# Performance work log

Hardware: AMD Instinct MI355X
Metric: run time of the kernel (lower is better)

## Reference

```python
import jax, jax.numpy as jnp
import numpy as np

GROUPS = 32
EPS = 1e-6


def group_norm(x, gamma, beta):
    b, c, h, w = x.shape
    xg = x.reshape(b, GROUPS, c // GROUPS, h, w)
    mu = xg.mean(axis=(2, 3, 4), keepdims=True)
    var = xg.var(axis=(2, 3, 4), keepdims=True)
    xg = (xg - mu) * jax.lax.rsqrt(var + EPS)
    return xg.reshape(b, c, h, w) * gamma[None, :, None, None] + beta[None, :, None, None]


def conv1x1(x, W, b):
    # 1x1 conv == per-pixel channel GEMM
    return jnp.einsum('oc,bchw->bohw', W, x) + b[None, :, None, None]


def scores(h_, Wq, bq, Wk, bk):
    b, c, H, Wd = h_.shape
    n = H * Wd
    q = conv1x1(h_, Wq, bq).reshape(b, c, n)  # b c n
    k = conv1x1(h_, Wk, bk).reshape(b, c, n)
    # q rearranged to (b, n, c), k to (b, c, n): w_[b,i,j] = sum_c q[b,c,i] k[b,c,j]
    return jnp.einsum('bci,bcj->bij', q, k) * (c ** -0.5)


def proc_attention(v, w_, H, Wd, Wp, bp):
    # w_ already softmaxed over last dim (j). h_[b,c,k] = sum_j v[b,c,j] * w_[b,k,j]
    h_ = jnp.einsum('bkj,bcj->bck', w_, v)
    b, c, _ = h_.shape
    h_ = h_.reshape(b, c, H, Wd)
    return conv1x1(h_, Wp, bp)


def setup_inputs() -> dict:
    key = jax.random.key(0)
    ks = jax.random.split(key, 12)
    B, C, H, W = 8, 256, 48, 48
    s = C ** -0.5
    return {
        'x1': jax.random.normal(ks[0], (B, C, H, W), dtype=jnp.float32),
        'x2': jax.random.normal(ks[1], (B, C, H, W), dtype=jnp.float32),
        'gamma': jnp.ones((C,), jnp.float32),
        'beta': jnp.zeros((C,), jnp.float32),
        'Wq': jax.random.normal(ks[2], (C, C), jnp.float32) * s,
        'bq': jnp.zeros((C,), jnp.float32),
        'Wk': jax.random.normal(ks[3], (C, C), jnp.float32) * s,
        'bk': jnp.zeros((C,), jnp.float32),
        'Wv': jax.random.normal(ks[4], (C, C), jnp.float32) * s,
        'bv': jnp.zeros((C,), jnp.float32),
        'Wp': jax.random.normal(ks[5], (C, C), jnp.float32) * s,
        'bp': jnp.zeros((C,), jnp.float32),
    }


def reference(x1, x2, gamma, beta, Wq, bq, Wk, bk, Wv, bv, Wp, bp):
    b, c, H, Wd = x1.shape
    h1n = group_norm(x1, gamma, beta)
    w1 = scores(h1n, Wq, bq, Wk, bk)                       # [b, n, n]
    v = conv1x1(h1n, Wv, bv).reshape(b, c, H * Wd)          # [b, c, n]
    out_self = x1 + proc_attention(v, jax.nn.softmax(w1, axis=-1), H, Wd, Wp, bp)
    h2n = group_norm(x2, gamma, beta)
    w2 = scores(h2n, Wq, bq, Wk, bk)
    out_cross = x1 + proc_attention(v, jax.nn.softmax(w1 + w2, axis=-1), H, Wd, Wp, bp)
    return (out_self, out_cross)
```

## Files before the change

### kernel.cpp

```cpp
#include <hip/hip_runtime.h>
#include <stdint.h>

typedef unsigned short ushort_t;
typedef __attribute__((ext_vector_type(8))) short bf16x8;
typedef __attribute__((ext_vector_type(4))) float f32x4;
typedef __attribute__((ext_vector_type(16))) float f32x16;
typedef __attribute__((ext_vector_type(4))) unsigned short us4;

static __device__ __forceinline__ unsigned short f2bf(float f) {
  union { float f; uint32_t u; } v; v.f = f;
  uint32_t u = v.u;
  u += 0x7FFFu + ((u >> 16) & 1u);
  return (unsigned short)(u >> 16);
}

static __device__ __forceinline__ float wredsum(float v) {
#pragma unroll
  for (int o = 32; o > 0; o >>= 1) v += __shfl_down(v, o, 64);
  return v;
}

__global__ __launch_bounds__(256) void cvt_w(
    const float* __restrict__ Wq, const float* __restrict__ Wk,
    const float* __restrict__ Wv, const float* __restrict__ Wp,
    ushort_t* __restrict__ dst) {
  int m = blockIdx.y;
  const float* src = (m == 0) ? Wq : (m == 1) ? Wk : (m == 2) ? Wv : Wp;
  int i = blockIdx.x * 256 + threadIdx.x;
  float4 v = ((const float4*)src)[i];
  us4 o;
  o.x = f2bf(v.x); o.y = f2bf(v.y); o.z = f2bf(v.z); o.w = f2bf(v.w);
  *(us4*)&dst[(size_t)m * 65536 + (size_t)i * 4] = o;
}

__global__ __launch_bounds__(512) void pack_bqk(const float* __restrict__ bq,
                                                const float* __restrict__ bk,
                                                float* __restrict__ bqk) {
  int i = threadIdx.x;
  bqk[i] = (i < 256) ? bq[i] : bk[i - 256];
}

__global__ __launch_bounds__(256) void gn_stats(
    const float* __restrict__ x1, const float* __restrict__ x2,
    float* __restrict__ stats) {
  const int sel = blockIdx.x >> 8;
  const int bg = blockIdx.x & 255;
  const float* x = (sel ? x2 : x1) + (size_t)bg * 8 * 2304;
  float s = 0.f, ss = 0.f;
  for (int i = threadIdx.x; i < 4608; i += 256) {
    float4 v = ((const float4*)x)[i];
    s += v.x + v.y + v.z + v.w;
    ss += v.x * v.x + v.y * v.y + v.z * v.z + v.w * v.w;
  }
  s = wredsum(s);
  ss = wredsum(ss);
  __shared__ float ls[8];
  int wave = threadIdx.x >> 6, lane = threadIdx.x & 63;
  if (lane == 0) { ls[wave] = s; ls[4 + wave] = ss; }
  __syncthreads();
  if (threadIdx.x == 0) {
    float S = ls[0] + ls[1] + ls[2] + ls[3];
    float SS = ls[4] + ls[5] + ls[6] + ls[7];
    float mu = S * (1.f / 18432.f);
    float var = SS * (1.f / 18432.f) - mu * mu;
    stats[(sel * 256 + bg) * 2] = mu;
    stats[(sel * 256 + bg) * 2 + 1] = rsqrtf(var + 1e-6f);
  }
}

__global__ __launch_bounds__(256) void gn_apply(
    const float* __restrict__ x1, const float* __restrict__ x2,
    const float* __restrict__ gamma, const float* __restrict__ beta,
    const float* __restrict__ stats,
    ushort_t* __restrict__ h1t, ushort_t* __restrict__ h2t) {
  const int sel = blockIdx.z, b = blockIdx.y, nt = blockIdx.x;
  const int n0 = nt * 64;
  const float* x = (sel ? x2 : x1) + (size_t)b * 256 * 2304;
  ushort_t* ht = (sel ? h2t : h1t) + (size_t)b * 2304 * 256;
  const float* st = stats + (sel * 8 + b) * 64;
  __shared__ ushort_t lt[64 * 260];
#pragma unroll 4
  for (int it = 0; it < 64; ++it) {
    int flat = it * 256 + threadIdx.x;
    int c = flat >> 6, nn = flat & 63;
    float v = x[(size_t)c * 2304 + n0 + nn];
    int g = c >> 3;
    float mu = st[g * 2], rstd = st[g * 2 + 1];
    lt[nn * 260 + c] = f2bf((v - mu) * rstd * gamma[c] + beta[c]);
  }
  __syncthreads();
#pragma unroll 4
  for (int it = 0; it < 16; ++it) {
    int flat4 = it * 256 + threadIdx.x;
    int nn = flat4 >> 6, cq = flat4 & 63;
    us4 vv = *(const us4*)&lt[nn * 260 + cq * 4];
    *(us4*)&ht[(size_t)(n0 + nn) * 256 + cq * 4] = vv;
  }
}

template <int MODE_OUT>
__global__ __launch_bounds__(256) void gemm_bt(
    const ushort_t* __restrict__ Av, const ushort_t* __restrict__ Bv,
    void* __restrict__ Cv, int M, int N, int K, long sA, long sB, long sC,
    const float* __restrict__ bias, const float* __restrict__ res, long sRes,
    void* __restrict__ Cv2) {
  __shared__ ushort_t lA[128 * 32];
  __shared__ ushort_t lB[128 * 32];
  const int tid = threadIdx.x;
  const int lane = tid & 63, wave = tid >> 6;
  const int wm = wave >> 1, wn = wave & 1;
  const int bz = blockIdx.z;
  const int bM = blockIdx.x * 128, bN = blockIdx.y * 128;

  const ushort_t* B = Bv + (size_t)bz * sB + (size_t)bN * K;
  const ushort_t* Ab = Av + (size_t)bz * sA + (size_t)bM * K;

  f32x4 acc[4][4];
#pragma unroll
  for (int m = 0; m < 4; ++m)
#pragma unroll
    for (int n = 0; n < 4; ++n) acc[m][n] = (f32x4){0.f, 0.f, 0.f, 0.f};

  const int nK = K >> 5;
  for (int kt = 0; kt < nK; ++kt) {
    __syncthreads();
#pragma unroll
    for (int i = 0; i < 2; ++i) {
      int c = i * 256 + tid;
      int row = c >> 2, cb = (c & 3) * 8;
      const ushort_t* src = B + (size_t)row * K + kt * 32 + cb;
      __builtin_amdgcn_global_load_lds(
          (const __attribute__((address_space(1))) uint32_t*)src,
          (__attribute__((address_space(3))) uint32_t*)((char*)lB + i * 4096 +
                                                        wave * 1024),
          16, 0, 0);
    }
#pragma unroll
    for (int i = 0; i < 2; ++i) {
      int c = i * 256 + tid;
      int row = c >> 2, cb = (c & 3) * 8;
      const ushort_t* src = Ab + (size_t)row * K + kt * 32 + cb;
      __builtin_amdgcn_global_load_lds(
          (const __attribute__((address_space(1))) uint32_t*)src,
          (__attribute__((address_space(3))) uint32_t*)((char*)lA + i * 4096 +
                                                        wave * 1024),
          16, 0, 0);
    }
    __syncthreads();

    bf16x8 af[4], bfr[4];
    const int ko = (lane >> 4) * 8;
    const int rb = lane & 15;
#pragma unroll
    for (int m = 0; m < 4; ++m)
      af[m] = *(const bf16x8*)&lA[(wm * 64 + m * 16 + rb) * 32 + ko];
#pragma unroll
    for (int n = 0; n < 4; ++n)
      bfr[n] = *(const bf16x8*)&lB[(wn * 64 + n * 16 + rb) * 32 + ko];
#pragma unroll
    for (int m = 0; m < 4; ++m)
#pragma unroll
      for (int n = 0; n < 4; ++n)
        acc[m][n] =
            __builtin_amdgcn_mfma_f32_16x16x32_bf16(af[m], bfr[n], acc[m][n],
                                                    0, 0, 0);
  }

  const int r0 = (lane >> 4) * 4;
  const int c0 = lane & 15;
#pragma unroll
  for (int m = 0; m < 4; ++m) {
#pragma unroll
    for (int n = 0; n < 4; ++n) {
#pragma unroll
      for (int j = 0; j < 4; ++j) {
        int row = bM + wm * 64 + m * 16 + r0 + j;
        int col = bN + wn * 64 + n * 16 + c0;
        float v = acc[m][n][j];
        size_t idx = (size_t)row * N + col;
        if (MODE_OUT == 0) {
          ((ushort_t*)Cv + (size_t)bz * sC)[idx] = f2bf(v + bias[col]);
        } else if (MODE_OUT == 1) {
          ((ushort_t*)Cv + (size_t)bz * sC)[idx] = f2bf(v + bias[row]);
        } else if (MODE_OUT == 5) {
          ((float*)Cv + (size_t)bz * sC)[idx] =
              v + bias[row] + (res + (size_t)bz * sRes)[idx];
        } else if (MODE_OUT == 6) {
          float vv = v + bias[col];
          if (col < 256) {
            ((ushort_t*)Cv + (size_t)bz * sC)[(size_t)row * 256 + col] =
                f2bf(vv);
          } else {
            int cp = col - 256;
            size_t kidx = (size_t)(row >> 6) * 16384 + (size_t)(cp >> 3) * 512 +
                          (size_t)(row & 63) * 8 + (cp & 7);
            ((ushort_t*)Cv2 + (size_t)bz * 589824)[kidx] = f2bf(vv);
          }
        } else if (MODE_OUT == 7) {
          size_t vidx = (size_t)(col >> 6) * 16384 +
                        (size_t)((col >> 3) & 7) * 2048 + (size_t)row * 8 +
                        (col & 7);
          ((ushort_t*)Cv + (size_t)bz * sC)[vidx] = f2bf(v + bias[row]);
        }
      }
    }
  }
}

__global__ __launch_bounds__(256, 2) void flash_attn(
    const ushort_t* __restrict__ q1t, const ushort_t* __restrict__ kf1,
    const ushort_t* __restrict__ q2t, const ushort_t* __restrict__ kf2,
    const ushort_t* __restrict__ vf, ushort_t* __restrict__ att1,
    ushort_t* __restrict__ att2) {
  const int bid = blockIdx.x;
  const int b = bid & 7;
  const int qb = bid >> 3;
  const int tid = threadIdx.x;
  const int lane = tid & 63;
  const int w = tid >> 6;
  const int grp = w >> 1;
  const int wp = w & 1;
  const int l31 = lane & 31;
  const int h = lane >> 5;

  const size_t sH = (size_t)2304 * 256;
  const ushort_t* qp0 = (grp ? q2t : q1t) + b * sH;
  const bf16x8* kb = (const bf16x8*)((grp ? kf2 : kf1) + b * sH);
  const bf16x8* vb = (const bf16x8*)(vf + b * sH);

  __shared__ ushort_t P1[2][32 * 64];
  __shared__ ushort_t P12[32 * 64];
  __shared__ float S1[32 * 64];
  __shared__ float red[2][32];

  bf16x8 qf[16];
  {
    const ushort_t* qp = qp0 + (size_t)(qb * 32 + l31) * 256 + h * 8;
#pragma unroll
    for (int ck = 0; ck < 16; ++ck) qf[ck] = *(const bf16x8*)(qp + ck * 16);
  }

  f32x16 o[4];
#pragma unroll
  for (int cb = 0; cb < 4; ++cb)
#pragma unroll
    for (int r = 0; r < 16; ++r) o[cb][r] = 0.f;
  float lp = 0.f;
  const int iswz = (l31 & 7) << 4;

  auto do_pv = [&](int tt) {
    const ushort_t* pb = grp ? P12 : P1[tt & 1];
    const bf16x8* vt = vb + (size_t)tt * 2048;
#pragma unroll
    for (int jc = 0; jc < 4; ++jc) {
      bf16x8 pa = *(const bf16x8*)((const char*)pb +
                                   ((l31 * 128 + jc * 32 + h * 16) ^ iswz));
#pragma unroll
      for (int cb = 0; cb < 4; ++cb) {
        bf16x8 vfr = vt[(jc * 2 + h) * 256 + wp * 128 + cb * 32 + l31];
        o[cb] =
            __builtin_amdgcn_mfma_f32_32x32x16_bf16(pa, vfr, o[cb], 0, 0, 0);
      }
    }
  };

  f32x16 s2save;
  for (int t = 0; t < 36; ++t) {
    f32x16 s;
#pragma unroll
    for (int r = 0; r < 16; ++r) s[r] = 0.f;
    {
      const bf16x8* kt = kb + (size_t)t * 2048 + wp * 32 + l31;
#pragma unroll
      for (int ck = 0; ck < 16; ++ck) {
        bf16x8 kf = kt[(ck * 2 + h) * 64];
        s = __builtin_amdgcn_mfma_f32_32x32x16_bf16(kf, qf[ck], s, 0, 0, 0);
      }
    }
    if (t > 0) do_pv(t - 1);
    if (grp == 0) {
      float e[16];
#pragma unroll
      for (int r = 0; r < 16; ++r) {
        e[r] = __expf(s[r] * 0.0625f - 8.f);
        lp += e[r];
      }
      char* p1 = (char*)P1[t & 1];
      char* s1 = (char*)S1;
#pragma unroll
      for (int g = 0; g < 4; ++g) {
        uint32_t u0 = (uint32_t)f2bf(e[4 * g]) |
                      ((uint32_t)f2bf(e[4 * g + 1]) << 16);
        uint32_t u1 = (uint32_t)f2bf(e[4 * g + 2]) |
                      ((uint32_t)f2bf(e[4 * g + 3]) << 16);
        *(uint2*)(p1 + ((l31 * 128 + wp * 64 + g * 16 + h * 8) ^ iswz)) =
            make_uint2(u0, u1);
        float4 sv = make_float4(s[4 * g], s[4 * g + 1], s[4 * g + 2],
                                s[4 * g + 3]);
        *(float4*)(s1 + ((l31 * 256 + wp * 128 + g * 32 + h * 16) ^ iswz)) =
            sv;
      }
    } else {
      s2save = s;
    }
    __syncthreads();
    if (grp == 1) {
      const char* s1 = (const char*)S1;
      char* p12 = (char*)P12;
#pragma unroll
      for (int g = 0; g < 4; ++g) {
        float4 sv = *(const float4*)(s1 + ((l31 * 256 + wp * 128 + g * 32 +
                                            h * 16) ^ iswz));
        float e0 = __expf((sv.x + s2save[4 * g + 0]) * 0.0625f - 8.f);
        float e1 = __expf((sv.y + s2save[4 * g + 1]) * 0.0625f - 8.f);
        float e2 = __expf((sv.z + s2save[4 * g + 2]) * 0.0625f - 8.f);
        float e3 = __expf((sv.w + s2save[4 * g + 3]) * 0.0625f - 8.f);
        lp += e0 + e1 + e2 + e3;
        uint32_t u0 = (uint32_t)f2bf(e0) | ((uint32_t)f2bf(e1) << 16);
        uint32_t u1 = (uint32_t)f2bf(e2) | ((uint32_t)f2bf(e3) << 16);
        *(uint2*)(p12 + ((l31 * 128 + wp * 64 + g * 16 + h * 8) ^ iswz)) =
            make_uint2(u0, u1);
      }
    }
    __syncthreads();
  }
  do_pv(35);

  lp += __shfl_xor(lp, 32, 64);
  __syncthreads();
  if (wp == 0 && lane < 32) red[grp][l31] = lp;
  __syncthreads();
  if (wp == 1 && lane < 32) red[grp][l31] += lp;
  __syncthreads();

  ushort_t* ap = (grp ? att2 : att1) + ((size_t)b * 2304 + qb * 32) * 256;
#pragma unroll
  for (int r = 0; r < 16; ++r) {
    int irow = (r & 3) + 8 * (r >> 2) + 4 * h;
    float rl = 1.f / red[grp][irow];
#pragma unroll
    for (int cb = 0; cb < 4; ++cb) {
      int col = wp * 128 + cb * 32 + l31;
      ap[(size_t)irow * 256 + col] = f2bf(o[cb][r] * rl);
    }
  }
}

extern "C" void kernel_launch(void* const* d_in, const int* in_sizes, int n_in,
                              void* d_out, int out_size, void* d_ws,
                              size_t ws_size, hipStream_t stream) {
  (void)in_sizes; (void)n_in; (void)out_size; (void)ws_size;
  const float* x1 = (const float*)d_in[0];
  const float* x2 = (const float*)d_in[1];
  const float* gamma = (const float*)d_in[2];
  const float* beta = (const float*)d_in[3];
  const float* Wq = (const float*)d_in[4];
  const float* bq = (const float*)d_in[5];
  const float* Wk = (const float*)d_in[6];
  const float* bk = (const float*)d_in[7];
  const float* Wv = (const float*)d_in[8];
  const float* bv = (const float*)d_in[9];
  const float* Wp = (const float*)d_in[10];
  const float* bp = (const float*)d_in[11];
  float* out = (float*)d_out;

  const int C = 256, N = 2304;
  const long sH = (long)N * C;
  const long sX = (long)C * N;
  const size_t HE = (size_t)8 * N * C;

  char* ws = (char*)d_ws;
  ushort_t* Wbf = (ushort_t*)ws;
  float* stats = (float*)(ws + 524288);
  float* bqk = (float*)(ws + 528384);
  ushort_t* h1t = (ushort_t*)(ws + 532480);
  ushort_t* h2t = h1t + HE;
  ushort_t* q1t = h2t + HE;
  ushort_t* q2t = q1t + HE;
  ushort_t* kf1 = q2t + HE;
  ushort_t* kf2 = kf1 + HE;
  ushort_t* vfB = kf2 + HE;
  ushort_t* att1 = vfB + HE;
  ushort_t* att2 = att1 + HE;

  cvt_w<<<dim3(64, 4), 256, 0, stream>>>(Wq, Wk, Wv, Wp, Wbf);
  pack_bqk<<<1, 512, 0, stream>>>(bq, bk, bqk);
  gn_stats<<<512, 256, 0, stream>>>(x1, x2, stats);
  gn_apply<<<dim3(36, 8, 2), 256, 0, stream>>>(x1, x2, gamma, beta, stats, h1t,
                                               h2t);

  gemm_bt<6><<<dim3(18, 4, 8), 256, 0, stream>>>(h1t, Wbf, q1t, N, 512, C, sH,
                                                 0, sH, bqk, nullptr, 0, kf1);
  gemm_bt<6><<<dim3(18, 4, 8), 256, 0, stream>>>(h2t, Wbf, q2t, N, 512, C, sH,
                                                 0, sH, bqk, nullptr, 0, kf2);
  gemm_bt<7><<<dim3(2, 18, 8), 256, 0, stream>>>(Wbf + 2 * 65536, h1t, vfB, C,
                                                 N, C, 0, sH, sH, bv, nullptr,
                                                 0, nullptr);

  flash_attn<<<576, 256, 0, stream>>>(q1t, kf1, q2t, kf2, vfB, att1, att2);

  const size_t half = (size_t)8 * C * N;
  gemm_bt<5><<<dim3(2, 18, 8), 256, 0, stream>>>(Wbf + 3 * 65536, att1, out, C,
                                                 N, C, 0, sH, sX, bp, x1, sX,
                                                 nullptr);
  gemm_bt<5><<<dim3(2, 18, 8), 256, 0, stream>>>(Wbf + 3 * 65536, att2,
                                                 out + half, C, N, C, 0, sH,
                                                 sX, bp, x1, sX, nullptr);
}
```

Before: 511.6 us.

## Split self and cross attention into separate blocks, recomputing S1 for cross

Each flash-attention block now handles only one group (self or cross). Cross blocks recompute the self scores by accumulating both QK^T products into one accumulator, with Q2 staged in swizzled shared memory. This removes the shared-memory S1 exchange and one barrier per tile, and doubles the block count at 128 threads each. In exchange, cross blocks do twice the QK MFMA work and read K1 and K2, while self blocks finish earlier, so the two block types are imbalanced.

```diff
diff --git a/kernel.cpp b/kernel.cpp
--- a/kernel.cpp
+++ b/kernel.cpp
@@ -207,38 +207,49 @@
   }
 }
 
-__global__ __launch_bounds__(256, 2) void flash_attn(
+__global__ __launch_bounds__(128, 3) void flash_attn(
     const ushort_t* __restrict__ q1t, const ushort_t* __restrict__ kf1,
     const ushort_t* __restrict__ q2t, const ushort_t* __restrict__ kf2,
     const ushort_t* __restrict__ vf, ushort_t* __restrict__ att1,
     ushort_t* __restrict__ att2) {
   const int bid = blockIdx.x;
   const int b = bid & 7;
-  const int qb = bid >> 3;
+  const int grp = (bid >> 3) & 1;
+  const int qb = bid >> 4;
   const int tid = threadIdx.x;
   const int lane = tid & 63;
-  const int w = tid >> 6;
-  const int grp = w >> 1;
-  const int wp = w & 1;
+  const int wp = tid >> 6;
   const int l31 = lane & 31;
   const int h = lane >> 5;
 
   const size_t sH = (size_t)2304 * 256;
-  const ushort_t* qp0 = (grp ? q2t : q1t) + b * sH;
-  const bf16x8* kb = (const bf16x8*)((grp ? kf2 : kf1) + b * sH);
+  const bf16x8* kb1 = (const bf16x8*)(kf1 + b * sH);
+  const bf16x8* kb2 = (const bf16x8*)(kf2 + b * sH);
   const bf16x8* vb = (const bf16x8*)(vf + b * sH);
 
-  __shared__ ushort_t P1[2][32 * 64];
-  __shared__ ushort_t P12[32 * 64];
-  __shared__ float S1[32 * 64];
-  __shared__ float red[2][32];
+  __shared__ ushort_t P[2][32 * 64];
+  __shared__ ushort_t q2l[32 * 256];
+  __shared__ float red[32];
+
+  if (grp == 1) {
+    int r = tid >> 2, qq = tid & 3;
+    const ushort_t* src =
+        q2t + b * sH + (size_t)(qb * 32 + r) * 256 + qq * 64;
+#pragma unroll
+    for (int k = 0; k < 8; ++k) {
+      bf16x8 v = *(const bf16x8*)(src + k * 8);
+      int cbyte = (qq * 128 + k * 16) ^ ((r & 15) << 4);
+      *(bf16x8*)((char*)q2l + r * 512 + cbyte) = v;
+    }
+  }
 
   bf16x8 qf[16];
   {
-    const ushort_t* qp = qp0 + (size_t)(qb * 32 + l31) * 256 + h * 8;
+    const ushort_t* qp = q1t + b * sH + (size_t)(qb * 32 + l31) * 256 + h * 8;
 #pragma unroll
     for (int ck = 0; ck < 16; ++ck) qf[ck] = *(const bf16x8*)(qp + ck * 16);
   }
+  __syncthreads();
 
   f32x16 o[4];
 #pragma unroll
@@ -249,7 +260,7 @@
   const int iswz = (l31 & 7) << 4;
 
   auto do_pv = [&](int tt) {
-    const ushort_t* pb = grp ? P12 : P1[tt & 1];
+    const ushort_t* pb = P[tt & 1];
     const bf16x8* vt = vb + (size_t)tt * 2048;
 #pragma unroll
     for (int jc = 0; jc < 4; ++jc) {
@@ -264,61 +275,41 @@
     }
   };
 
-  f32x16 s2save;
   for (int t = 0; t < 36; ++t) {
     f32x16 s;
 #pragma unroll
     for (int r = 0; r < 16; ++r) s[r] = 0.f;
+    if (grp == 1) {
+      const bf16x8* kt2 = kb2 + (size_t)t * 2048 + wp * 32 + l31;
+#pragma unroll
+      for (int ck = 0; ck < 16; ++ck) {
+        bf16x8 kf = kt2[(ck * 2 + h) * 64];
+        int cbyte = (ck * 32 + h * 16) ^ ((l31 & 15) << 4);
+        bf16x8 q2f = *(const bf16x8*)((const char*)q2l + l31 * 512 + cbyte);
+        s = __builtin_amdgcn_mfma_f32_32x32x16_bf16(kf, q2f, s, 0, 0, 0);
+      }
+    }
     {
-      const bf16x8* kt = kb + (size_t)t * 2048 + wp * 32 + l31;
+      const bf16x8* kt1 = kb1 + (size_t)t * 2048 + wp * 32 + l31;
 #pragma unroll
       for (int ck = 0; ck < 16; ++ck) {
-        bf16x8 kf = kt[(ck * 2 + h) * 64];
+        bf16x8 kf = kt1[(ck * 2 + h) * 64];
         s = __builtin_amdgcn_mfma_f32_32x32x16_bf16(kf, qf[ck], s, 0, 0, 0);
       }
     }
     if (t > 0) do_pv(t - 1);
-    if (grp == 0) {
-      float e[16];
-#pragma unroll
-      for (int r = 0; r < 16; ++r) {
-        e[r] = __expf(s[r] * 0.0625f - 8.f);
-        lp += e[r];
-      }
-      char* p1 = (char*)P1[t & 1];
-      char* s1 = (char*)S1;
+    {
+      char* p = (char*)P[t & 1];
 #pragma unroll
       for (int g = 0; g < 4; ++g) {
-        uint32_t u0 = (uint32_t)f2bf(e[4 * g]) |
-                      ((uint32_t)f2bf(e[4 * g + 1]) << 16);
-        uint32_t u1 = (uint32_t)f2bf(e[4 * g + 2]) |
-                      ((uint32_t)f2bf(e[4 * g + 3]) << 16);
-        *(uint2*)(p1 + ((l31 * 128 + wp * 64 + g * 16 + h * 8) ^ iswz)) =
-            make_uint2(u0, u1);
-        float4 sv = make_float4(s[4 * g], s[4 * g + 1], s[4 * g + 2],
-                                s[4 * g + 3]);
-        *(float4*)(s1 + ((l31 * 256 + wp * 128 + g * 32 + h * 16) ^ iswz)) =
-            sv;
-      }
-    } else {
-      s2save = s;
-    }
-    __syncthreads();
-    if (grp == 1) {
-      const char* s1 = (const char*)S1;
-      char* p12 = (char*)P12;
-#pragma unroll
-      for (int g = 0; g < 4; ++g) {
-        float4 sv = *(const float4*)(s1 + ((l31 * 256 + wp * 128 + g * 32 +
-                                            h * 16) ^ iswz));
-        float e0 = __expf((sv.x + s2save[4 * g + 0]) * 0.0625f - 8.f);
-        float e1 = __expf((sv.y + s2save[4 * g + 1]) * 0.0625f - 8.f);
-        float e2 = __expf((sv.z + s2save[4 * g + 2]) * 0.0625f - 8.f);
-        float e3 = __expf((sv.w + s2save[4 * g + 3]) * 0.0625f - 8.f);
+        float e0 = __expf(s[4 * g + 0] * 0.0625f - 8.f);
+        float e1 = __expf(s[4 * g + 1] * 0.0625f - 8.f);
+        float e2 = __expf(s[4 * g + 2] * 0.0625f - 8.f);
+        float e3 = __expf(s[4 * g + 3] * 0.0625f - 8.f);
         lp += e0 + e1 + e2 + e3;
         uint32_t u0 = (uint32_t)f2bf(e0) | ((uint32_t)f2bf(e1) << 16);
         uint32_t u1 = (uint32_t)f2bf(e2) | ((uint32_t)f2bf(e3) << 16);
-        *(uint2*)(p12 + ((l31 * 128 + wp * 64 + g * 16 + h * 8) ^ iswz)) =
+        *(uint2*)(p + ((l31 * 128 + wp * 64 + g * 16 + h * 8) ^ iswz)) =
             make_uint2(u0, u1);
       }
     }
@@ -327,17 +318,16 @@
   do_pv(35);
 
   lp += __shfl_xor(lp, 32, 64);
-  __syncthreads();
-  if (wp == 0 && lane < 32) red[grp][l31] = lp;
-  __syncthreads();
-  if (wp == 1 && lane < 32) red[grp][l31] += lp;
+  if (wp == 0 && lane < 32) red[l31] = lp;
+  __syncthreads();
+  if (wp == 1 && lane < 32) red[l31] += lp;
   __syncthreads();
 
   ushort_t* ap = (grp ? att2 : att1) + ((size_t)b * 2304 + qb * 32) * 256;
 #pragma unroll
   for (int r = 0; r < 16; ++r) {
     int irow = (r & 3) + 8 * (r >> 2) + 4 * h;
-    float rl = 1.f / red[grp][irow];
+    float rl = 1.f / red[irow];
 #pragma unroll
     for (int cb = 0; cb < 4; ++cb) {
       int col = wp * 128 + cb * 32 + l31;
@@ -397,7 +387,7 @@
                                                  N, C, 0, sH, sH, bv, nullptr,
                                                  0, nullptr);
 
-  flash_attn<<<576, 256, 0, stream>>>(q1t, kf1, q2t, kf2, vfB, att1, att2);
+  flash_attn<<<1152, 128, 0, stream>>>(q1t, kf1, q2t, kf2, vfB, att1, att2);
 
   const size_t half = (size_t)8 * C * N;
   gemm_bt<5><<<dim3(2, 18, 8), 256, 0, stream>>>(Wbf + 3 * 65536, att1, out, C,
```

New measurement: 875.1 us. 71.1% more time.
